# Performance work log

Measured on AMD Instinct MI355X. Metric: run time of the kernel, lower is better.

## Reference

```python
import jax, jax.numpy as jnp
import numpy as np

N_NODES = 50000
N_EDGES = 800000
H = 128
CHEM_DIM = 34   # 2 + 2*num_gdf
GEOM_DIM = 48   # 2*num_gdf + num_signatures
EPS = 1e-5


def _linear_params(key, d_in, d_out):
    kw, kb = jax.random.split(key)
    lim = 1.0 / np.sqrt(d_in)
    w = jax.random.uniform(kw, (d_in, d_out), jnp.float32, -lim, lim)
    b = jax.random.uniform(kb, (d_out,), jnp.float32, -lim, lim)
    return w, b


def setup_inputs() -> dict:
    key = jax.random.key(0)
    ks = jax.random.split(key, 16)
    inp = {
        'chem_feats': jax.random.normal(ks[0], (N_EDGES, CHEM_DIM), jnp.float32),
        'geom_feats': jax.random.normal(ks[1], (N_NODES, GEOM_DIM), jnp.float32),
        'nbr_vids': jax.random.randint(ks[2], (N_EDGES,), 0, N_NODES, jnp.int32),
    }
    # chem_mlp: Linear(34,128) -> BN(128) -> SiLU -> Linear(128,256) -> BN(256)
    inp['w_c1'], inp['b_c1'] = _linear_params(ks[3], CHEM_DIM, H)
    inp['g_c1'], inp['be_c1'] = jnp.ones((H,), jnp.float32), jnp.zeros((H,), jnp.float32)
    inp['w_c2'], inp['b_c2'] = _linear_params(ks[4], H, 2 * H)
    inp['g_c2'], inp['be_c2'] = jnp.ones((2 * H,), jnp.float32), jnp.zeros((2 * H,), jnp.float32)
    # geom_mlp: Linear(48,64) -> BN(64) -> SiLU -> Linear(64,64) -> BN(64)
    inp['w_g1'], inp['b_g1'] = _linear_params(ks[5], GEOM_DIM, H // 2)
    inp['g_g1'], inp['be_g1'] = jnp.ones((H // 2,), jnp.float32), jnp.zeros((H // 2,), jnp.float32)
    inp['w_g2'], inp['b_g2'] = _linear_params(ks[6], H // 2, H // 2)
    inp['g_g2'], inp['be_g2'] = jnp.ones((H // 2,), jnp.float32), jnp.zeros((H // 2,), jnp.float32)
    # feat_mlp: Linear(192,128) -> BN(128) -> SiLU -> Linear(128,128) -> BN(128)
    inp['w_f1'], inp['b_f1'] = _linear_params(ks[7], H + H // 2, H)
    inp['g_f1'], inp['be_f1'] = jnp.ones((H,), jnp.float32), jnp.zeros((H,), jnp.float32)
    inp['w_f2'], inp['b_f2'] = _linear_params(ks[8], H, H)
    inp['g_f2'], inp['be_f2'] = jnp.ones((H,), jnp.float32), jnp.zeros((H,), jnp.float32)
    return inp


def _bn(x, gamma, beta):
    # BatchNorm1d with batch statistics (training-mode normalization; dropout = identity at eval)
    m = jnp.mean(x, axis=0)
    v = jnp.var(x, axis=0)
    return gamma * (x - m) * jax.lax.rsqrt(v + EPS) + beta


def reference(chem_feats, geom_feats, nbr_vids,
              w_c1, b_c1, g_c1, be_c1, w_c2, b_c2, g_c2, be_c2,
              w_g1, b_g1, g_g1, be_g1, w_g2, b_g2, g_g2, be_g2,
              w_f1, b_f1, g_f1, be_f1, w_f2, b_f2, g_f2, be_f2):
    # chem branch: per-edge MLP
    h = _bn(chem_feats @ w_c1 + b_c1, g_c1, be_c1)
    h = jax.nn.silu(h)
    h = _bn(h @ w_c2 + b_c2, g_c2, be_c2)            # [E, 2H]
    nbr_filter, nbr_core = jnp.split(h, 2, axis=-1)
    h_chem = jax.nn.sigmoid(nbr_filter) * jax.nn.softplus(nbr_core)  # [E, H]
    # scatter-sum per-edge features into node bins
    h_chem = jax.ops.segment_sum(h_chem, nbr_vids, num_segments=N_NODES)  # [N, H]
    # geom branch: per-node MLP
    hg = _bn(geom_feats @ w_g1 + b_g1, g_g1, be_g1)
    hg = jax.nn.silu(hg)
    h_geom = _bn(hg @ w_g2 + b_g2, g_g2, be_g2)      # [N, H/2]
    # fuse
    hf = jnp.concatenate((h_chem, h_geom), axis=-1)  # [N, 3H/2]
    hf = _bn(hf @ w_f1 + b_f1, g_f1, be_f1)
    hf = jax.nn.silu(hf)
    h_out = _bn(hf @ w_f2 + b_f2, g_f2, be_f2)       # [N, H]
    return h_out
```

## Files before the change

### kernel.cpp

```cpp
#include <hip/hip_runtime.h>
#include <hip/hip_bf16.h>
#include <cmath>

#define E_EDGES 800000
#define N_NODES 50000
#define BN_EPS 1e-5f

typedef __attribute__((ext_vector_type(8))) short short8;
typedef __attribute__((ext_vector_type(4))) float float4v;
typedef __attribute__((ext_vector_type(4))) unsigned int uint4v;
typedef unsigned short ushort_t;

#define MFMA16(a, b, c) __builtin_amdgcn_mfma_f32_16x16x32_bf16((a), (b), (c), 0, 0, 0)

#define OFF_GX 0
#define OFF_GH 2304
#define OFF_A1 23040
#define OFF_C1 23168
#define OFF_A2 23296
#define OFF_C2 23552
#define OFF_GS1SUM 23808
#define OFF_GS1SQ 23872
#define OFF_GS2SUM 23936
#define OFF_GS2SQ 24000
#define OFF_FS1SUM 24064
#define OFF_FS1SQ 24192
#define OFF_FS2SUM 24320
#define OFF_FS2SQ 24448
#define OFF_NODE 24576
#define OFF_TG2 (OFF_NODE + N_NODES * 128)
#define OFF_TF1 (OFF_TG2 + N_NODES * 64)
#define OFF_TF2 OFF_NODE
#define OFF_W1T (OFF_TF1 + N_NODES * 128)
#define OFF_W2T (OFF_W1T + 4096)
#define OFF_BASEI (OFF_W2T + 16384)
#define OFF_BTOT (OFF_BASEI + 50176)
#define OFF_CNT (OFF_BTOT + 256)
#define OFF_CUR (OFF_CNT + 50176)
#define OFF_SIDX (OFF_CUR + 50176)
#define OFF_VIDS (OFF_SIDX + E_EDGES)
#define OFF_HLIN (OFF_VIDS + E_EDGES)

__device__ __forceinline__ float frcp_(float x) { return __builtin_amdgcn_rcpf(x); }
__device__ __forceinline__ float sigmoid_(float x) { return frcp_(1.0f + __expf(-x)); }
__device__ __forceinline__ float softplus_(float x) {
  return (x > 20.0f) ? x : __logf(1.0f + __expf(x));
}
__device__ __forceinline__ float silu_(float x) { return x * frcp_(1.0f + __expf(-x)); }

__device__ __forceinline__ ushort_t f2bf(float f) {
  __hip_bfloat16 h = __float2bfloat16(f);
  return *(ushort_t*)&h;
}
__device__ __forceinline__ float bf2f(ushort_t u) {
  return __uint_as_float(((unsigned)u) << 16);
}
__device__ __forceinline__ unsigned cvtpk(float lo, float hi) {
  unsigned r;
  asm("v_cvt_pk_bf16_f32 %0, %1, %2" : "=v"(r) : "v"(lo), "v"(hi));
  return r;
}
__device__ __forceinline__ void gload_lds16(const void* g, void* l) {
  __builtin_amdgcn_global_load_lds(
      (const __attribute__((address_space(1))) unsigned int*)g,
      (__attribute__((address_space(3))) unsigned int*)l, 16, 0, 0);
}

__device__ __forceinline__ void load_xfrag(const float* __restrict__ chem, int e, int qd,
                                           short8* x0, short8* x1) {
  const float* xe = chem + e * 34;
  float2 p0 = *(const float2*)(xe + 8 * qd);
  float2 p1 = *(const float2*)(xe + 8 * qd + 2);
  float2 p2 = *(const float2*)(xe + 8 * qd + 4);
  float2 p3 = *(const float2*)(xe + 8 * qd + 6);
  union { short8 s; uint4v u; } cv;
  cv.u[0] = cvtpk(p0.x, p0.y);
  cv.u[1] = cvtpk(p1.x, p1.y);
  cv.u[2] = cvtpk(p2.x, p2.y);
  cv.u[3] = cvtpk(p3.x, p3.y);
  *x0 = cv.s;
  union { short8 s; uint4v u; } cb;
  cb.u = (uint4v){0, 0, 0, 0};
  if (qd == 0) {
    float2 pt = *(const float2*)(xe + 32);
    cb.u[0] = cvtpk(pt.x, pt.y);
  }
  *x1 = cb.s;
}

__global__ __launch_bounds__(256) void k_prep(const float* __restrict__ w1,
                                              const float* __restrict__ w2,
                                              float* __restrict__ ws) {
  ushort_t* w1t = (ushort_t*)(ws + OFF_W1T);
  ushort_t* w2t = (ushort_t*)(ws + OFF_W2T);
  int idx = blockIdx.x * 256 + threadIdx.x;
  if (idx < 128 * 64) {
    int c = idx >> 6, k = idx & 63;
    float v = (k < 34) ? w1[k * 128 + c] : 0.0f;
    w1t[idx] = f2bf(v);
  }
  int j = idx - 128 * 64;
  if (j >= 0 && j < 256 * 128) {
    int c = j >> 7, k = j & 127;
    w2t[j] = f2bf(w2[k * 256 + c]);
  }
}

__global__ __launch_bounds__(256) void k_hist(const int* __restrict__ vids,
                                              float* __restrict__ ws) {
  const int e = blockIdx.x * 256 + threadIdx.x;
  int* cnt = (int*)(ws + OFF_CNT);
  if (e < E_EDGES) atomicAdd(&cnt[vids[e]], 1);
}

__global__ __launch_bounds__(256) void k_scan1(float* __restrict__ ws) {
  const int* cnt = (const int*)(ws + OFF_CNT);
  int* base = (int*)(ws + OFF_BASEI);
  int* btot = (int*)(ws + OFF_BTOT);
  const int t = threadIdx.x, b = blockIdx.x, i = b * 256 + t;
  const int lane = t & 63, w = t >> 6;
  int c = (i < N_NODES) ? cnt[i] : 0;
  int s = c;
#pragma unroll
  for (int o = 1; o < 64; o <<= 1) {
    int y = __shfl_up(s, o);
    if (lane >= o) s += y;
  }
  __shared__ int wsum[4];
  if (lane == 63) wsum[w] = s;
  __syncthreads();
  int add = 0;
#pragma unroll
  for (int k = 0; k < 4; ++k)
    if (k < w) add += wsum[k];
  base[i] = s + add - c;
  if (t == 255) btot[b] = s + add;
}

__global__ __launch_bounds__(256) void k_scan2(float* __restrict__ ws) {
  int* btot = (int*)(ws + OFF_BTOT);
  const int t = threadIdx.x;
  const int lane = t & 63, w = t >> 6;
  int c = (t < 196) ? btot[t] : 0;
  int s = c;
#pragma unroll
  for (int o = 1; o < 64; o <<= 1) {
    int y = __shfl_up(s, o);
    if (lane >= o) s += y;
  }
  __shared__ int wsum[4];
  if (lane == 63) wsum[w] = s;
  __syncthreads();
  int add = 0;
#pragma unroll
  for (int k = 0; k < 4; ++k)
    if (k < w) add += wsum[k];
  if (t < 196) btot[t] = s + add - c;
}

__global__ __launch_bounds__(256) void k_fill(const int* __restrict__ vids,
                                              float* __restrict__ ws) {
  const int e = blockIdx.x * 256 + threadIdx.x;
  const int* base = (const int*)(ws + OFF_BASEI);
  const int* btot = (const int*)(ws + OFF_BTOT);
  int* cur = (int*)(ws + OFF_CUR);
  int* sidx = (int*)(ws + OFF_SIDX);
  int* vsrt = (int*)(ws + OFF_VIDS);
  if (e < E_EDGES) {
    int v = vids[e];
    int pos = base[v] + btot[v >> 8] + atomicAdd(&cur[v], 1);
    sidx[pos] = e;
    vsrt[pos] = v;
  }
}

__global__ __launch_bounds__(256) void k_xstats(const float* __restrict__ chem,
                                                float* __restrict__ ws) {
  __shared__ __align__(16) ushort_t xT[2][48 * 72];
  const int t = threadIdx.x, wv = t >> 6, ln = t & 63, r15 = ln & 15, qd = ln >> 4;
  for (int i = t; i < 2 * 14 * 72; i += 256) {
    int b = i / (14 * 72), j = i % (14 * 72);
    int rr = j / 72, e = j % 72;
    xT[b][(34 + rr) * 72 + e] = (rr == 0 && e < 64) ? (ushort_t)0x3F80 : (ushort_t)0;
  }
  float4v g0 = {0, 0, 0, 0}, g1 = {0, 0, 0, 0};
#pragma unroll 2
  for (int it = 0; it < 10; ++it) {
    const int st = blockIdx.x * 10 + it;
    const int buf = it & 1;
    for (int i = t; i < 64 * 17; i += 256) {
      int e = i / 17, kp = i - e * 17;
      float2 v = *(const float2*)(chem + st * 2176 + e * 34 + 2 * kp);
      unsigned u = cvtpk(v.x, v.y);
      xT[buf][(2 * kp) * 72 + e] = (ushort_t)u;
      xT[buf][(2 * kp + 1) * 72 + e] = (ushort_t)(u >> 16);
    }
    __syncthreads();
    const ushort_t* xb = &xT[buf][0];
#pragma unroll
    for (int ks = 0; ks < 2; ++ks) {
      const ushort_t* xk = xb + ks * 32 + 8 * qd;
      short8 f0 = *(const short8*)&xk[(0 + r15) * 72];
      short8 f1 = *(const short8*)&xk[(16 + r15) * 72];
      short8 f2v = *(const short8*)&xk[(32 + r15) * 72];
      if (wv == 0) { g0 = MFMA16(f0, f0, g0); g1 = MFMA16(f0, f1, g1); }
      else if (wv == 1) { g0 = MFMA16(f0, f2v, g0); g1 = MFMA16(f1, f1, g1); }
      else if (wv == 2) { g0 = MFMA16(f1, f2v, g0); }
      else { g0 = MFMA16(f2v, f2v, g0); }
    }
  }
  float* GX = ws + OFF_GX;
  int ti0, tj0, ti1 = -1, tj1 = -1;
  if (wv == 0) { ti0 = 0; tj0 = 0; ti1 = 0; tj1 = 1; }
  else if (wv == 1) { ti0 = 0; tj0 = 2; ti1 = 1; tj1 = 1; }
  else if (wv == 2) { ti0 = 1; tj0 = 2; }
  else { ti0 = 2; tj0 = 2; }
#pragma unroll
  for (int r = 0; r < 4; ++r)
    atomicAdd(&GX[(16 * ti0 + 4 * qd + r) * 48 + 16 * tj0 + r15], g0[r]);
  if (ti1 >= 0)
#pragma unroll
    for (int r = 0; r < 4; ++r)
      atomicAdd(&GX[(16 * ti1 + 4 * qd + r) * 48 + 16 * tj1 + r15], g1[r]);
}

__global__ __launch_bounds__(64) void k_bn1(const float* __restrict__ b1,
                                            const float* __restrict__ g1,
                                            const float* __restrict__ be1,
                                            float* __restrict__ ws) {
  const int c = blockIdx.x, i = threadIdx.x;
  __shared__ float wc[34];
  const ushort_t* w1t = (const ushort_t*)(ws + OFF_W1T);
  const float* GX = ws + OFF_GX;
  if (i < 34) wc[i] = bf2f(w1t[c * 64 + i]);
  __syncthreads();
  float p = 0.0f, ps = 0.0f;
  if (i < 34) {
    float gi = 0.0f;
    for (int j = 0; j < 34; ++j) {
      int a = i, b = j;
      if ((a >> 4) > (b >> 4)) { int tt = a; a = b; b = tt; }
      gi += GX[a * 48 + b] * wc[j];
    }
    p = wc[i] * gi;
    ps = wc[i] * GX[i * 48 + 34];
  }
#pragma unroll
  for (int off = 1; off < 64; off <<= 1) {
    p += __shfl_xor(p, off);
    ps += __shfl_xor(ps, off);
  }
  if (i == 0) {
    const float E = (float)E_EDGES;
    float bc = b1[c];
    float sum = ps + E * bc;
    float sq = p + 2.0f * bc * ps + E * bc * bc;
    float m = sum / E, v = sq / E - m * m;
    float a = g1[c] * rsqrtf(v + BN_EPS);
    ws[OFF_A1 + c] = a;
    ws[OFF_C1 + c] = a * (bc - m) + be1[c];
  }
}

template <int TJA, int TJB>
__device__ __forceinline__ void ghstep(const ushort_t* hk, int r15, float4v (&g)[11]) {
  short8 f[TJB + 1];
#pragma unroll
  for (int i = 0; i <= TJB; ++i) f[i] = *(const short8*)&hk[(16 * i + r15) * 72];
  short8 f8 = *(const short8*)&hk[(128 + r15) * 72];
  int s = 0;
#pragma unroll
  for (int ti = 0; ti <= TJA; ++ti) { g[s] = MFMA16(f[ti], f[TJA], g[s]); ++s; }
  g[s] = MFMA16(f8, f[TJA], g[s]); ++s;
#pragma unroll
  for (int ti = 0; ti <= TJB; ++ti) { g[s] = MFMA16(f[ti], f[TJB], g[s]); ++s; }
  g[s] = MFMA16(f8, f[TJB], g[s]);
}

__device__ __forceinline__ void ghtile(float* GH, int ti, int tj, int r15, int qd,
                                       const float4v v) {
#pragma unroll
  for (int r = 0; r < 4; ++r)
    atomicAdd(&GH[(16 * ti + 4 * qd + r) * 144 + 16 * tj + r15], v[r]);
}

template <int TJA, int TJB>
__device__ __forceinline__ void ghflush(float* GH, int r15, int qd, const float4v (&g)[11]) {
  int s = 0;
#pragma unroll
  for (int ti = 0; ti <= TJA; ++ti) { ghtile(GH, ti, TJA, r15, qd, g[s]); ++s; }
  ghtile(GH, 8, TJA, r15, qd, g[s]); ++s;
#pragma unroll
  for (int ti = 0; ti <= TJB; ++ti) { ghtile(GH, ti, TJB, r15, qd, g[s]); ++s; }
  ghtile(GH, 8, TJB, r15, qd, g[s]);
}

__global__ __launch_bounds__(256) void k_h(const float* __restrict__ chem,
                                           float* __restrict__ ws, int store_h) {
  __shared__ __align__(16) ushort_t hT[2][144 * 72];
  const int t = threadIdx.x, wv = t >> 6, ln = t & 63, r15 = ln & 15, qd = ln >> 4;
  const ushort_t* w1t = (const ushort_t*)(ws + OFF_W1T);
  for (int i = t; i < 2 * 16 * 72; i += 256) {
    int b = i / (16 * 72), j = i % (16 * 72);
    int rr = j / 72, e = j % 72;
    hT[b][(128 + rr) * 72 + e] = (rr == 0 && e < 64) ? (ushort_t)0x3F80 : (ushort_t)0;
  }
  float a1c[2], c1c[2];
#pragma unroll
  for (int cf = 0; cf < 2; ++cf) {
    int col = 32 * wv + 16 * cf + r15;
    a1c[cf] = ws[OFF_A1 + col];
    c1c[cf] = ws[OFF_C1 + col];
  }
  float4v gacc[11];
#pragma unroll
  for (int s = 0; s < 11; ++s) gacc[s] = (float4v){0, 0, 0, 0};

#pragma unroll 2
  for (int it = 0; it < 10; ++it) {
    const int st = blockIdx.x * 10 + it;
    const int buf = it & 1;
    const int e_base = st * 64;
    short8 xa0[4], xa1[4];
#pragma unroll
    for (int rb = 0; rb < 4; ++rb)
      load_xfrag(chem, e_base + 16 * rb + r15, qd, &xa0[rb], &xa1[rb]);
#pragma unroll
    for (int cf = 0; cf < 2; ++cf) {
      const int col = 32 * wv + 16 * cf + r15;
      short8 wb0 = *(const short8*)&w1t[col * 64 + 8 * qd];
      short8 wb1 = *(const short8*)&w1t[col * 64 + 32 + 8 * qd];
#pragma unroll
      for (int rb = 0; rb < 4; ++rb) {
        float4v acc = (float4v){0, 0, 0, 0};
        acc = MFMA16(xa0[rb], wb0, acc);
        acc = MFMA16(xa1[rb], wb1, acc);
        float h0 = silu_(fmaf(a1c[cf], acc[0], c1c[cf]));
        float h1 = silu_(fmaf(a1c[cf], acc[1], c1c[cf]));
        float h2 = silu_(fmaf(a1c[cf], acc[2], c1c[cf]));
        float h3 = silu_(fmaf(a1c[cf], acc[3], c1c[cf]));
        unsigned lo = cvtpk(h0, h1), hi = cvtpk(h2, h3);
        unsigned long long pk = ((unsigned long long)hi << 32) | (unsigned long long)lo;
        *(unsigned long long*)&hT[buf][col * 72 + 16 * rb + 4 * qd] = pk;
      }
    }
    __syncthreads();
    if (store_h) {
      unsigned* hlin = (unsigned*)(ws + OFF_HLIN);
      const int e_loc = t >> 2, qq = t & 3;
      const ushort_t* hb2 = &hT[buf][0];
      unsigned* dst = hlin + (size_t)(e_base + e_loc) * 64 + 16 * qq;
#pragma unroll
      for (int jj = 0; jj < 4; ++jj) {
        uint4v o;
#pragma unroll
        for (int m = 0; m < 4; ++m) {
          int u = 16 * qq + 4 * jj + m;
          unsigned lo = hb2[(2 * u) * 72 + e_loc];
          unsigned hi = hb2[(2 * u + 1) * 72 + e_loc];
          o[m] = lo | (hi << 16);
        }
        *(uint4v*)(dst + 4 * jj) = o;
      }
    }
    const ushort_t* hb = &hT[buf][0];
#pragma unroll
    for (int ks = 0; ks < 2; ++ks) {
      const ushort_t* hk = hb + ks * 32 + 8 * qd;
      if (wv == 0) ghstep<0, 7>(hk, r15, gacc);
      else if (wv == 1) ghstep<1, 6>(hk, r15, gacc);
      else if (wv == 2) ghstep<2, 5>(hk, r15, gacc);
      else ghstep<3, 4>(hk, r15, gacc);
    }
  }
  float* GH = ws + OFF_GH;
  if (wv == 0) ghflush<0, 7>(GH, r15, qd, gacc);
  else if (wv == 1) ghflush<1, 6>(GH, r15, qd, gacc);
  else if (wv == 2) ghflush<2, 5>(GH, r15, qd, gacc);
  else ghflush<3, 4>(GH, r15, qd, gacc);
}

__global__ __launch_bounds__(128) void k_bn2(const float* __restrict__ b2,
                                             const float* __restrict__ g2,
                                             const float* __restrict__ be2,
                                             float* __restrict__ ws) {
  const int c = blockIdx.x, i = threadIdx.x;
  __shared__ float wcol[128];
  __shared__ float redQ[2], redS[2];
  const ushort_t* w2t = (const ushort_t*)(ws + OFF_W2T);
  const float* GH = ws + OFF_GH;
  wcol[i] = bf2f(w2t[c * 128 + i]);
  __syncthreads();
  float wi = wcol[i];
  float gi = 0.0f;
  for (int j = 0; j < 128; ++j) {
    int a = i, b = j;
    if ((a >> 4) > (b >> 4)) { int tt = a; a = b; b = tt; }
    gi += GH[a * 144 + b] * wcol[j];
  }
  float p = wi * gi;
  float ps = wi * GH[128 * 144 + i];
#pragma unroll
  for (int off = 1; off < 64; off <<= 1) {
    p += __shfl_xor(p, off);
    ps += __shfl_xor(ps, off);
  }
  const int wv = i >> 6, ln = i & 63;
  if (ln == 0) { redQ[wv] = p; redS[wv] = ps; }
  __syncthreads();
  if (i == 0) {
    float q = redQ[0] + redQ[1], s = redS[0] + redS[1];
    const float E = (float)E_EDGES;
    float bc = b2[c];
    float sum = s + E * bc;
    float sq = q + 2.0f * bc * s + E * bc * bc;
    float m = sum / E, v = sq / E - m * m;
    float a = g2[c] * rsqrtf(v + BN_EPS);
    ws[OFF_A2 + c] = a;
    ws[OFF_C2 + c] = a * (bc - m) + be2[c];
  }
}

__global__ __launch_bounds__(256) void k_scatter(float* __restrict__ ws) {
  __shared__ __align__(16) ushort_t hS[64 * 128];
  __shared__ __align__(16) float gS[64 * 133];
  __shared__ int vS[64];
  const int t = threadIdx.x, wv = t >> 6, ln = t & 63, r15 = ln & 15, qd = ln >> 4;
  const ushort_t* w2t = (const ushort_t*)(ws + OFF_W2T);
  const int* sidx = (const int*)(ws + OFF_SIDX);
  const int* vsrt = (const int*)(ws + OFF_VIDS);
  const unsigned* hlin = (const unsigned*)(ws + OFF_HLIN);
  float* node = ws + OFF_NODE;
  float aF2[2], cF2[2], aC2[2], cC2[2];
#pragma unroll
  for (int cf = 0; cf < 2; ++cf) {
    int col = 32 * wv + 16 * cf + r15;
    aF2[cf] = ws[OFF_A2 + col];
    cF2[cf] = ws[OFF_C2 + col];
    aC2[cf] = ws[OFF_A2 + 128 + col];
    cC2[cf] = ws[OFF_C2 + 128 + col];
  }
  const int st0 = blockIdx.x * 8;
  int eid_cur = 0, vid_cur = 0;
  if (st0 < 12500) { eid_cur = sidx[st0 * 64 + ln]; vid_cur = vsrt[st0 * 64 + ln]; }
  for (int it = 0; it < 8; ++it) {
    const int st = st0 + it;
    if (st >= 12500) break;
    int eid_nxt = 0, vid_nxt = 0;
    if (it < 7 && st + 1 < 12500) {
      eid_nxt = sidx[(st + 1) * 64 + ln];
      vid_nxt = vsrt[(st + 1) * 64 + ln];
    }
#pragma unroll
    for (int k = 0; k < 4; ++k) {
      const int row = 16 * wv + 4 * k + qd;
      const int er = __shfl(eid_cur, row);
      const int c = (ln & 15) ^ (row & 15);
      gload_lds16(hlin + (size_t)er * 64 + 4 * c, (void*)&hS[(16 * wv + 4 * k) * 128]);
    }
    __syncthreads();
    if (t < 64) vS[t] = vid_cur;
    short8 hf[4][4];
#pragma unroll
    for (int ks = 0; ks < 4; ++ks)
#pragma unroll
      for (int rb = 0; rb < 4; ++rb)
        hf[ks][rb] = *(const short8*)&hS[(16 * rb + r15) * 128 + ((4 * ks + qd) ^ r15) * 8];
#pragma unroll
    for (int cf = 0; cf < 2; ++cf) {
      const int colF = 32 * wv + 16 * cf + r15;
      float4v accF[4], accC[4];
#pragma unroll
      for (int rb = 0; rb < 4; ++rb) {
        accF[rb] = (float4v){0, 0, 0, 0};
        accC[rb] = (float4v){0, 0, 0, 0};
      }
#pragma unroll
      for (int ks = 0; ks < 4; ++ks) {
        short8 bF = *(const short8*)&w2t[colF * 128 + ks * 32 + 8 * qd];
        short8 bC = *(const short8*)&w2t[(128 + colF) * 128 + ks * 32 + 8 * qd];
#pragma unroll
        for (int rb = 0; rb < 4; ++rb) {
          accF[rb] = MFMA16(hf[ks][rb], bF, accF[rb]);
          accC[rb] = MFMA16(hf[ks][rb], bC, accC[rb]);
        }
      }
#pragma unroll
      for (int rb = 0; rb < 4; ++rb)
#pragma unroll
        for (int r = 0; r < 4; ++r) {
          float F = fmaf(aF2[cf], accF[rb][r], cF2[cf]);
          float Co = fmaf(aC2[cf], accC[rb][r], cC2[cf]);
          gS[(16 * rb + 4 * qd + r) * 133 + colF] = sigmoid_(F) * softplus_(Co);
        }
    }
    __syncthreads();
    {
      const int c = t & 127, half = t >> 7;
      const float* g = &gS[(32 * half) * 133 + c];
      const int* vv = &vS[32 * half];
      float acc = g[0];
      int vcur = vv[0];
#pragma unroll
      for (int r = 1; r < 32; ++r) {
        int v = vv[r];
        float x = g[r * 133];
        if (v != vcur) {
          atomicAdd(node + (size_t)vcur * 128 + c, acc);
          acc = 0.0f;
          vcur = v;
        }
        acc += x;
      }
      atomicAdd(node + (size_t)vcur * 128 + c, acc);
    }
    eid_cur = eid_nxt;
    vid_cur = vid_nxt;
  }
}

__global__ __launch_bounds__(256) void k_scatter_fb(const float* __restrict__ chem,
                                                    float* __restrict__ ws) {
  __shared__ __align__(16) ushort_t hS[64 * 136];
  __shared__ __align__(16) float gS[64 * 133];
  __shared__ int vS[64];
  const int t = threadIdx.x, wv = t >> 6, ln = t & 63, r15 = ln & 15, qd = ln >> 4;
  const ushort_t* w1t = (const ushort_t*)(ws + OFF_W1T);
  const ushort_t* w2t = (const ushort_t*)(ws + OFF_W2T);
  const int* sidx = (const int*)(ws + OFF_SIDX);
  const int* vsrt = (const int*)(ws + OFF_VIDS);
  float* node = ws + OFF_NODE;
  float a1c[2], c1c[2], aF2[2], cF2[2], aC2[2], cC2[2];
#pragma unroll
  for (int cf = 0; cf < 2; ++cf) {
    int col = 32 * wv + 16 * cf + r15;
    a1c[cf] = ws[OFF_A1 + col];
    c1c[cf] = ws[OFF_C1 + col];
    aF2[cf] = ws[OFF_A2 + col];
    cF2[cf] = ws[OFF_C2 + col];
    aC2[cf] = ws[OFF_A2 + 128 + col];
    cC2[cf] = ws[OFF_C2 + 128 + col];
  }
  for (int it = 0; it < 8; ++it) {
    const int st = blockIdx.x * 8 + it;
    if (st >= 12500) break;
    const int e_base = st * 64;
    const int myeid = sidx[e_base + ln];
    const int myvid = vsrt[e_base + ln];
    short8 xa0[4], xa1[4];
#pragma unroll
    for (int rb = 0; rb < 4; ++rb) {
      int er = __shfl(myeid, 16 * rb + r15);
      load_xfrag(chem, er, qd, &xa0[rb], &xa1[rb]);
    }
#pragma unroll
    for (int cf = 0; cf < 2; ++cf) {
      const int col = 32 * wv + 16 * cf + r15;
      short8 wb0 = *(const short8*)&w1t[col * 64 + 8 * qd];
      short8 wb1 = *(const short8*)&w1t[col * 64 + 32 + 8 * qd];
#pragma unroll
      for (int rb = 0; rb < 4; ++rb) {
        float4v acc = (float4v){0, 0, 0, 0};
        acc = MFMA16(xa0[rb], wb0, acc);
        acc = MFMA16(xa1[rb], wb1, acc);
#pragma unroll
        for (int r = 0; r < 4; ++r) {
          float hv = silu_(fmaf(a1c[cf], acc[r], c1c[cf]));
          hS[(16 * rb + 4 * qd + r) * 136 + col] = (ushort_t)cvtpk(hv, hv);
        }
      }
    }
    __syncthreads();
    if (t < 64) vS[t] = myvid;
#pragma unroll
    for (int cf = 0; cf < 2; ++cf) {
      const int colF = 32 * wv + 16 * cf + r15;
      float4v accF[4], accC[4];
#pragma unroll
      for (int rb = 0; rb < 4; ++rb) {
        accF[rb] = (float4v){0, 0, 0, 0};
        accC[rb] = (float4v){0, 0, 0, 0};
      }
#pragma unroll
      for (int ks = 0; ks < 4; ++ks) {
        short8 bF = *(const short8*)&w2t[colF * 128 + ks * 32 + 8 * qd];
        short8 bC = *(const short8*)&w2t[(128 + colF) * 128 + ks * 32 + 8 * qd];
#pragma unroll
        for (int rb = 0; rb < 4; ++rb) {
          short8 hf = *(const short8*)&hS[(16 * rb + r15) * 136 + ks * 32 + 8 * qd];
          accF[rb] = MFMA16(hf, bF, accF[rb]);
          accC[rb] = MFMA16(hf, bC, accC[rb]);
        }
      }
#pragma unroll
      for (int rb = 0; rb < 4; ++rb)
#pragma unroll
        for (int r = 0; r < 4; ++r) {
          float F = fmaf(aF2[cf], accF[rb][r], cF2[cf]);
          float Co = fmaf(aC2[cf], accC[rb][r], cC2[cf]);
          gS[(16 * rb + 4 * qd + r) * 133 + colF] = sigmoid_(F) * softplus_(Co);
        }
    }
    __syncthreads();
    {
      const int c = t & 127, half = t >> 7;
      const float* g = &gS[(32 * half) * 133 + c];
      const int* vv = &vS[32 * half];
      float acc = g[0];
      int vcur = vv[0];
#pragma unroll
      for (int r = 1; r < 32; ++r) {
        int v = vv[r];
        float x = g[r * 133];
        if (v != vcur) {
          atomicAdd(node + (size_t)vcur * 128 + c, acc);
          acc = 0.0f;
          vcur = v;
        }
        acc += x;
      }
      atomicAdd(node + (size_t)vcur * 128 + c, acc);
    }
  }
}

__global__ __launch_bounds__(256) void k_geom_stats1(const float* __restrict__ geom,
                                                     const float* __restrict__ wg1,
                                                     const float* __restrict__ bg1,
                                                     float* __restrict__ ws) {
  __shared__ float ssum[64], ssq[64];
  const int t = threadIdx.x, lane = t & 63, w = t >> 6;
  if (t < 64) { ssum[t] = 0.0f; ssq[t] = 0.0f; }
  __syncthreads();
  const float bcol = bg1[lane];
  const int nb = blockIdx.x * 16 + w * 4;
  float x[4], acc[4];
#pragma unroll
  for (int u = 0; u < 4; u++) {
    x[u] = (lane < 48) ? geom[(nb + u) * 48 + lane] : 0.0f;
    acc[u] = bcol;
  }
#pragma unroll 16
  for (int k = 0; k < 48; k++) {
    float wvv = wg1[k * 64 + lane];
#pragma unroll
    for (int u = 0; u < 4; u++) acc[u] = fmaf(__shfl(x[u], k), wvv, acc[u]);
  }
  float bs = 0.0f, bq = 0.0f;
#pragma unroll
  for (int u = 0; u < 4; u++) { bs += acc[u]; bq += acc[u] * acc[u]; }
  atomicAdd(&ssum[lane], bs);
  atomicAdd(&ssq[lane], bq);
  __syncthreads();
  if (t < 64) {
    atomicAdd(ws + OFF_GS1SUM + t, ssum[t]);
    atomicAdd(ws + OFF_GS1SQ + t, ssq[t]);
  }
}

__global__ __launch_bounds__(256) void k_geom_main(
    const float* __restrict__ geom, const float* __restrict__ wg1,
    const float* __restrict__ bg1, const float* __restrict__ gg1,
    const float* __restrict__ beg1, const float* __restrict__ wg2,
    const float* __restrict__ bg2, float* __restrict__ ws) {
  __shared__ float ssum[64], ssq[64];
  const int t = threadIdx.x, lane = t & 63, w = t >> 6;
  if (t < 64) { ssum[t] = 0.0f; ssq[t] = 0.0f; }
  const float invN = 1.0f / (float)N_NODES;
  float s1 = ws[OFF_GS1SUM + lane], q1 = ws[OFF_GS1SQ + lane];
  float m1 = s1 * invN, v1 = q1 * invN - m1 * m1;
  float a1 = gg1[lane] * rsqrtf(v1 + BN_EPS);
  float c1 = beg1[lane] - a1 * m1;
  const float bcol = bg1[lane], b2col = bg2[lane];
  __syncthreads();
  const int nb = blockIdx.x * 16 + w * 4;
  float x[4], tg1[4], hg[4], acc[4];
#pragma unroll
  for (int u = 0; u < 4; u++) {
    x[u] = (lane < 48) ? geom[(nb + u) * 48 + lane] : 0.0f;
    tg1[u] = bcol;
  }
#pragma unroll 16
  for (int k = 0; k < 48; k++) {
    float wvv = wg1[k * 64 + lane];
#pragma unroll
    for (int u = 0; u < 4; u++) tg1[u] = fmaf(__shfl(x[u], k), wvv, tg1[u]);
  }
#pragma unroll
  for (int u = 0; u < 4; u++) {
    hg[u] = silu_(fmaf(a1, tg1[u], c1));
    acc[u] = b2col;
  }
#pragma unroll 16
  for (int k = 0; k < 64; k++) {
    float wvv = wg2[k * 64 + lane];
#pragma unroll
    for (int u = 0; u < 4; u++) acc[u] = fmaf(__shfl(hg[u], k), wvv, acc[u]);
  }
  float bs = 0.0f, bq = 0.0f;
#pragma unroll
  for (int u = 0; u < 4; u++) {
    ws[OFF_TG2 + (nb + u) * 64 + lane] = acc[u];
    bs += acc[u]; bq += acc[u] * acc[u];
  }
  atomicAdd(&ssum[lane], bs);
  atomicAdd(&ssq[lane], bq);
  __syncthreads();
  if (t < 64) {
    atomicAdd(ws + OFF_GS2SUM + t, ssum[t]);
    atomicAdd(ws + OFF_GS2SQ + t, ssq[t]);
  }
}

__global__ __launch_bounds__(256) void k_fuse1(const float* __restrict__ wf1,
                                               const float* __restrict__ bf1,
                                               const float* __restrict__ gg2,
                                               const float* __restrict__ beg2,
                                               float* __restrict__ ws) {
  __shared__ float ssum[128], ssq[128];
  const int t = threadIdx.x, lane = t & 63, w = t >> 6;
  if (t < 128) { ssum[t] = 0.0f; ssq[t] = 0.0f; }
  const float invN = 1.0f / (float)N_NODES;
  float s2 = ws[OFF_GS2SUM + lane], q2 = ws[OFF_GS2SQ + lane];
  float mg = s2 * invN, vg = q2 * invN - mg * mg;
  float ag = gg2[lane] * rsqrtf(vg + BN_EPS);
  float cg_ = beg2[lane] - ag * mg;
  const float bA = bf1[lane], bB = bf1[64 + lane];
  __syncthreads();
  const int nb = blockIdx.x * 16 + w * 4;
  float xa[4], xb[4], xg[4], acc1[4], acc2[4];
#pragma unroll
  for (int u = 0; u < 4; u++) {
    int n = nb + u;
    xa[u] = ws[OFF_NODE + n * 128 + lane];
    xb[u] = ws[OFF_NODE + n * 128 + 64 + lane];
    xg[u] = fmaf(ag, ws[OFF_TG2 + n * 64 + lane], cg_);
    acc1[u] = bA; acc2[u] = bB;
  }
#pragma unroll 16
  for (int k = 0; k < 64; k++) {
    float w1v = wf1[k * 128 + lane], w2v = wf1[k * 128 + 64 + lane];
#pragma unroll
    for (int u = 0; u < 4; u++) {
      float xk = __shfl(xa[u], k);
      acc1[u] = fmaf(xk, w1v, acc1[u]);
      acc2[u] = fmaf(xk, w2v, acc2[u]);
    }
  }
#pragma unroll 16
  for (int k = 0; k < 64; k++) {
    float w1v = wf1[(64 + k) * 128 + lane], w2v = wf1[(64 + k) * 128 + 64 + lane];
#pragma unroll
    for (int u = 0; u < 4; u++) {
      float xk = __shfl(xb[u], k);
      acc1[u] = fmaf(xk, w1v, acc1[u]);
      acc2[u] = fmaf(xk, w2v, acc2[u]);
    }
  }
#pragma unroll 16
  for (int k = 0; k < 64; k++) {
    float w1v = wf1[(128 + k) * 128 + lane], w2v = wf1[(128 + k) * 128 + 64 + lane];
#pragma unroll
    for (int u = 0; u < 4; u++) {
      float xk = __shfl(xg[u], k);
      acc1[u] = fmaf(xk, w1v, acc1[u]);
      acc2[u] = fmaf(xk, w2v, acc2[u]);
    }
  }
  float sA = 0, qA = 0, sB = 0, qB = 0;
#pragma unroll
  for (int u = 0; u < 4; u++) {
    int n = nb + u;
    ws[OFF_TF1 + n * 128 + lane] = acc1[u];
    ws[OFF_TF1 + n * 128 + 64 + lane] = acc2[u];
    sA += acc1[u]; qA += acc1[u] * acc1[u];
    sB += acc2[u]; qB += acc2[u] * acc2[u];
  }
  atomicAdd(&ssum[lane], sA); atomicAdd(&ssq[lane], qA);
  atomicAdd(&ssum[64 + lane], sB); atomicAdd(&ssq[64 + lane], qB);
  __syncthreads();
  if (t < 128) {
    atomicAdd(ws + OFF_FS1SUM + t, ssum[t]);
    atomicAdd(ws + OFF_FS1SQ + t, ssq[t]);
  }
}

__global__ __launch_bounds__(256) void k_fuse2(const float* __restrict__ wf2,
                                               const float* __restrict__ bf2,
                                               const float* __restrict__ gf1,
                                               const float* __restrict__ bef1,
                                               float* __restrict__ ws) {
  __shared__ float ssum[128], ssq[128];
  const int t = threadIdx.x, lane = t & 63, w = t >> 6;
  if (t < 128) { ssum[t] = 0.0f; ssq[t] = 0.0f; }
  const float invN = 1.0f / (float)N_NODES;
  float sA_ = ws[OFF_FS1SUM + lane], qA_ = ws[OFF_FS1SQ + lane];
  float mA = sA_ * invN, vA = qA_ * invN - mA * mA;
  float aA = gf1[lane] * rsqrtf(vA + BN_EPS);
  float cA = bef1[lane] - aA * mA;
  float sB_ = ws[OFF_FS1SUM + 64 + lane], qB_ = ws[OFF_FS1SQ + 64 + lane];
  float mB = sB_ * invN, vB = qB_ * invN - mB * mB;
  float aB = gf1[64 + lane] * rsqrtf(vB + BN_EPS);
  float cB = bef1[64 + lane] - aB * mB;
  const float b1c = bf2[lane], b2c = bf2[64 + lane];
  __syncthreads();
  const int nb = blockIdx.x * 16 + w * 4;
  float ha[4], hb[4], acc1[4], acc2[4];
#pragma unroll
  for (int u = 0; u < 4; u++) {
    int n = nb + u;
    ha[u] = silu_(fmaf(aA, ws[OFF_TF1 + n * 128 + lane], cA));
    hb[u] = silu_(fmaf(aB, ws[OFF_TF1 + n * 128 + 64 + lane], cB));
    acc1[u] = b1c; acc2[u] = b2c;
  }
#pragma unroll 16
  for (int k = 0; k < 64; k++) {
    float w1v = wf2[k * 128 + lane], w2v = wf2[k * 128 + 64 + lane];
#pragma unroll
    for (int u = 0; u < 4; u++) {
      float xk = __shfl(ha[u], k);
      acc1[u] = fmaf(xk, w1v, acc1[u]);
      acc2[u] = fmaf(xk, w2v, acc2[u]);
    }
  }
#pragma unroll 16
  for (int k = 0; k < 64; k++) {
    float w1v = wf2[(64 + k) * 128 + lane], w2v = wf2[(64 + k) * 128 + 64 + lane];
#pragma unroll
    for (int u = 0; u < 4; u++) {
      float xk = __shfl(hb[u], k);
      acc1[u] = fmaf(xk, w1v, acc1[u]);
      acc2[u] = fmaf(xk, w2v, acc2[u]);
    }
  }
  float sA = 0, qA = 0, sB = 0, qB = 0;
#pragma unroll
  for (int u = 0; u < 4; u++) {
    int n = nb + u;
    ws[OFF_TF2 + n * 128 + lane] = acc1[u];
    ws[OFF_TF2 + n * 128 + 64 + lane] = acc2[u];
    sA += acc1[u]; qA += acc1[u] * acc1[u];
    sB += acc2[u]; qB += acc2[u] * acc2[u];
  }
  atomicAdd(&ssum[lane], sA); atomicAdd(&ssq[lane], qA);
  atomicAdd(&ssum[64 + lane], sB); atomicAdd(&ssq[64 + lane], qB);
  __syncthreads();
  if (t < 128) {
    atomicAdd(ws + OFF_FS2SUM + t, ssum[t]);
    atomicAdd(ws + OFF_FS2SQ + t, ssq[t]);
  }
}

__global__ __launch_bounds__(256) void k_final(const float* __restrict__ gf2,
                                               const float* __restrict__ bef2,
                                               const float* __restrict__ ws,
                                               float* __restrict__ out) {
  const int idx = blockIdx.x * 256 + threadIdx.x;
  const int base = idx * 4;
  if (base >= N_NODES * 128) return;
  const float invN = 1.0f / (float)N_NODES;
  const int c0 = base & 127;
  float4 v = *(const float4*)(ws + OFF_TF2 + base);
  float vv[4] = {v.x, v.y, v.z, v.w}, r[4];
#pragma unroll
  for (int j = 0; j < 4; j++) {
    int c = c0 + j;
    float s = ws[OFF_FS2SUM + c], q = ws[OFF_FS2SQ + c];
    float m = s * invN, var = q * invN - m * m;
    float a = gf2[c] * rsqrtf(var + BN_EPS);
    r[j] = fmaf(a, vv[j] - m, bef2[c]);
  }
  *(float4*)(out + base) = make_float4(r[0], r[1], r[2], r[3]);
}

extern "C" void kernel_launch(void* const* d_in, const int* in_sizes, int n_in,
                              void* d_out, int out_size, void* d_ws, size_t ws_size,
                              hipStream_t stream) {
  const float* chem = (const float*)d_in[0];
  const float* geom = (const float*)d_in[1];
  const int* vids = (const int*)d_in[2];
  const float* w_c1 = (const float*)d_in[3];  const float* b_c1 = (const float*)d_in[4];
  const float* g_c1 = (const float*)d_in[5];  const float* be_c1 = (const float*)d_in[6];
  const float* w_c2 = (const float*)d_in[7];  const float* b_c2 = (const float*)d_in[8];
  const float* g_c2 = (const float*)d_in[9];  const float* be_c2 = (const float*)d_in[10];
  const float* w_g1 = (const float*)d_in[11]; const float* b_g1 = (const float*)d_in[12];
  const float* g_g1 = (const float*)d_in[13]; const float* be_g1 = (const float*)d_in[14];
  const float* w_g2 = (const float*)d_in[15]; const float* b_g2 = (const float*)d_in[16];
  const float* g_g2 = (const float*)d_in[17]; const float* be_g2 = (const float*)d_in[18];
  const float* w_f1 = (const float*)d_in[19]; const float* b_f1 = (const float*)d_in[20];
  const float* g_f1 = (const float*)d_in[21]; const float* be_f1 = (const float*)d_in[22];
  const float* w_f2 = (const float*)d_in[23]; const float* b_f2 = (const float*)d_in[24];
  const float* g_f2 = (const float*)d_in[25]; const float* be_f2 = (const float*)d_in[26];
  float* ws = (float*)d_ws;
  float* out = (float*)d_out;

  const size_t need_ws = ((size_t)OFF_HLIN + (size_t)E_EDGES * 64) * sizeof(float);
  const int big = (ws_size >= need_ws) ? 1 : 0;

  hipMemsetAsync(d_ws, 0, (size_t)(OFF_NODE + N_NODES * 128) * sizeof(float), stream);
  hipMemsetAsync((void*)(ws + OFF_CNT), 0, (size_t)(2 * 50176) * sizeof(int), stream);

  k_prep<<<dim3(160), dim3(256), 0, stream>>>(w_c1, w_c2, ws);
  k_hist<<<dim3(3125), dim3(256), 0, stream>>>(vids, ws);
  k_scan1<<<dim3(196), dim3(256), 0, stream>>>(ws);
  k_scan2<<<dim3(1), dim3(256), 0, stream>>>(ws);
  k_fill<<<dim3(3125), dim3(256), 0, stream>>>(vids, ws);
  k_xstats<<<dim3(1250), dim3(256), 0, stream>>>(chem, ws);
  k_bn1<<<dim3(128), dim3(64), 0, stream>>>(b_c1, g_c1, be_c1, ws);
  k_h<<<dim3(1250), dim3(256), 0, stream>>>(chem, ws, big);
  k_bn2<<<dim3(256), dim3(128), 0, stream>>>(b_c2, g_c2, be_c2, ws);
  if (big) k_scatter<<<dim3(1563), dim3(256), 0, stream>>>(ws);
  else     k_scatter_fb<<<dim3(1563), dim3(256), 0, stream>>>(chem, ws);
  k_geom_stats1<<<dim3(3125), dim3(256), 0, stream>>>(geom, w_g1, b_g1, ws);
  k_geom_main<<<dim3(3125), dim3(256), 0, stream>>>(geom, w_g1, b_g1, g_g1, be_g1, w_g2, b_g2, ws);
  k_fuse1<<<dim3(3125), dim3(256), 0, stream>>>(w_f1, b_f1, g_g2, be_g2, ws);
  k_fuse2<<<dim3(3125), dim3(256), 0, stream>>>(w_f2, b_f2, g_f1, be_f1, ws);
  k_final<<<dim3(6250), dim3(256), 0, stream>>>(g_f2, be_f2, ws, out);
}
```

Measured before the change: 1.233 ms.

## Write first-layer activations in sorted order, stream them contiguously in scatter

k_h no longer stores the first-layer activations in edge order. A new k_sa kernel recomputes them from sorted edge indices and writes them in node-sorted order with an XOR-swizzled layout. k_sb then reads them with contiguous async LDS loads, double-prefetched, instead of per-edge gathers. The histogram is folded into k_xstats and k_hist is dropped. The cost is recomputing layer 1 and an extra launch and pass over the activation buffer; the gain is coalesced reads in the scatter stage and one fewer launch.

```diff
diff --git a/kernel.cpp b/kernel.cpp
--- a/kernel.cpp
+++ b/kernel.cpp
@@ -60,6 +60,11 @@
   asm("v_cvt_pk_bf16_f32 %0, %1, %2" : "=v"(r) : "v"(lo), "v"(hi));
   return r;
 }
+__device__ __forceinline__ void lds_barrier() {
+  asm volatile("s_waitcnt lgkmcnt(0)" ::: "memory");
+  __builtin_amdgcn_s_barrier();
+  asm volatile("" ::: "memory");
+}
 __device__ __forceinline__ void gload_lds16(const void* g, void* l) {
   __builtin_amdgcn_global_load_lds(
       (const __attribute__((address_space(1))) unsigned int*)g,
@@ -106,13 +111,6 @@
   }
 }
 
-__global__ __launch_bounds__(256) void k_hist(const int* __restrict__ vids,
-                                              float* __restrict__ ws) {
-  const int e = blockIdx.x * 256 + threadIdx.x;
-  int* cnt = (int*)(ws + OFF_CNT);
-  if (e < E_EDGES) atomicAdd(&cnt[vids[e]], 1);
-}
-
 __global__ __launch_bounds__(256) void k_scan1(float* __restrict__ ws) {
   const int* cnt = (const int*)(ws + OFF_CNT);
   int* base = (int*)(ws + OFF_BASEI);
@@ -175,9 +173,15 @@
 }
 
 __global__ __launch_bounds__(256) void k_xstats(const float* __restrict__ chem,
+                                                const int* __restrict__ vids,
                                                 float* __restrict__ ws) {
   __shared__ __align__(16) ushort_t xT[2][48 * 72];
   const int t = threadIdx.x, wv = t >> 6, ln = t & 63, r15 = ln & 15, qd = ln >> 4;
+  {
+    int* cnt = (int*)(ws + OFF_CNT);
+    const int e0 = blockIdx.x * 640;
+    for (int i = t; i < 640; i += 256) atomicAdd(&cnt[vids[e0 + i]], 1);
+  }
   for (int i = t; i < 2 * 14 * 72; i += 256) {
     int b = i / (14 * 72), j = i % (14 * 72);
     int rr = j / 72, e = j % 72;
@@ -296,7 +300,7 @@
 }
 
 __global__ __launch_bounds__(256) void k_h(const float* __restrict__ chem,
-                                           float* __restrict__ ws, int store_h) {
+                                           float* __restrict__ ws) {
   __shared__ __align__(16) ushort_t hT[2][144 * 72];
   const int t = threadIdx.x, wv = t >> 6, ln = t & 63, r15 = ln & 15, qd = ln >> 4;
   const ushort_t* w1t = (const ushort_t*)(ws + OFF_W1T);
@@ -345,24 +349,6 @@
       }
     }
     __syncthreads();
-    if (store_h) {
-      unsigned* hlin = (unsigned*)(ws + OFF_HLIN);
-      const int e_loc = t >> 2, qq = t & 3;
-      const ushort_t* hb2 = &hT[buf][0];
-      unsigned* dst = hlin + (size_t)(e_base + e_loc) * 64 + 16 * qq;
-#pragma unroll
-      for (int jj = 0; jj < 4; ++jj) {
-        uint4v o;
-#pragma unroll
-        for (int m = 0; m < 4; ++m) {
-          int u = 16 * qq + 4 * jj + m;
-          unsigned lo = hb2[(2 * u) * 72 + e_loc];
-          unsigned hi = hb2[(2 * u + 1) * 72 + e_loc];
-          o[m] = lo | (hi << 16);
-        }
-        *(uint4v*)(dst + 4 * jj) = o;
-      }
-    }
     const ushort_t* hb = &hT[buf][0];
 #pragma unroll
     for (int ks = 0; ks < 2; ++ks) {
@@ -421,13 +407,68 @@
   }
 }
 
-__global__ __launch_bounds__(256) void k_scatter(float* __restrict__ ws) {
+__global__ __launch_bounds__(256) void k_sa(const float* __restrict__ chem,
+                                            float* __restrict__ ws) {
+  __shared__ __align__(16) ushort_t hS[64 * 136];
+  const int t = threadIdx.x, wv = t >> 6, ln = t & 63, r15 = ln & 15, qd = ln >> 4;
+  const ushort_t* w1t = (const ushort_t*)(ws + OFF_W1T);
+  const int* sidx = (const int*)(ws + OFF_SIDX);
+  unsigned* hlin = (unsigned*)(ws + OFF_HLIN);
+  float a1c[2], c1c[2];
+#pragma unroll
+  for (int cf = 0; cf < 2; ++cf) {
+    int col = 32 * wv + 16 * cf + r15;
+    a1c[cf] = ws[OFF_A1 + col];
+    c1c[cf] = ws[OFF_C1 + col];
+  }
+  for (int it = 0; it < 4; ++it) {
+    const int st = blockIdx.x * 4 + it;
+    const int e_base = st * 64;
+    const int myeid = sidx[e_base + ln];
+    short8 xa0[4], xa1[4];
+#pragma unroll
+    for (int rb = 0; rb < 4; ++rb) {
+      int er = __shfl(myeid, 16 * rb + r15);
+      load_xfrag(chem, er, qd, &xa0[rb], &xa1[rb]);
+    }
+#pragma unroll
+    for (int cf = 0; cf < 2; ++cf) {
+      const int col = 32 * wv + 16 * cf + r15;
+      short8 wb0 = *(const short8*)&w1t[col * 64 + 8 * qd];
+      short8 wb1 = *(const short8*)&w1t[col * 64 + 32 + 8 * qd];
+#pragma unroll
+      for (int rb = 0; rb < 4; ++rb) {
+        float4v acc = (float4v){0, 0, 0, 0};
+        acc = MFMA16(xa0[rb], wb0, acc);
+        acc = MFMA16(xa1[rb], wb1, acc);
+#pragma unroll
+        for (int r = 0; r < 4; ++r) {
+          float hv = silu_(fmaf(a1c[cf], acc[r], c1c[cf]));
+          hS[(16 * rb + 4 * qd + r) * 136 + col] = (ushort_t)cvtpk(hv, hv);
+        }
+      }
+    }
+    lds_barrier();
+    {
+      const int lr = t >> 2;
+      unsigned* dst = hlin + (size_t)(e_base + lr) * 64;
+#pragma unroll
+      for (int j = 0; j < 4; ++j) {
+        const int c = 4 * (t & 3) + j;
+        uint4v v = *(const uint4v*)&hS[lr * 136 + 8 * c];
+        *(uint4v*)(dst + ((c ^ (lr & 15)) * 4)) = v;
+      }
+    }
+    lds_barrier();
+  }
+}
+
+__global__ __launch_bounds__(256) void k_sb(float* __restrict__ ws) {
   __shared__ __align__(16) ushort_t hS[64 * 128];
   __shared__ __align__(16) float gS[64 * 133];
   __shared__ int vS[64];
   const int t = threadIdx.x, wv = t >> 6, ln = t & 63, r15 = ln & 15, qd = ln >> 4;
   const ushort_t* w2t = (const ushort_t*)(ws + OFF_W2T);
-  const int* sidx = (const int*)(ws + OFF_SIDX);
   const int* vsrt = (const int*)(ws + OFF_VIDS);
   const unsigned* hlin = (const unsigned*)(ws + OFF_HLIN);
   float* node = ws + OFF_NODE;
@@ -441,31 +482,30 @@
     cC2[cf] = ws[OFF_C2 + 128 + col];
   }
   const int st0 = blockIdx.x * 8;
-  int eid_cur = 0, vid_cur = 0;
-  if (st0 < 12500) { eid_cur = sidx[st0 * 64 + ln]; vid_cur = vsrt[st0 * 64 + ln]; }
-  for (int it = 0; it < 8; ++it) {
-    const int st = st0 + it;
-    if (st >= 12500) break;
-    int eid_nxt = 0, vid_nxt = 0;
-    if (it < 7 && st + 1 < 12500) {
-      eid_nxt = sidx[(st + 1) * 64 + ln];
-      vid_nxt = vsrt[(st + 1) * 64 + ln];
-    }
-#pragma unroll
-    for (int k = 0; k < 4; ++k) {
-      const int row = 16 * wv + 4 * k + qd;
-      const int er = __shfl(eid_cur, row);
-      const int c = (ln & 15) ^ (row & 15);
-      gload_lds16(hlin + (size_t)er * 64 + 4 * c, (void*)&hS[(16 * wv + 4 * k) * 128]);
-    }
-    __syncthreads();
-    if (t < 64) vS[t] = vid_cur;
+  if (st0 >= 12500) return;
+  const int nt = (12500 - st0 < 8) ? (12500 - st0) : 8;
+#pragma unroll
+  for (int k = 0; k < 4; ++k)
+    gload_lds16(hlin + (size_t)(st0 * 64 + 16 * wv + 4 * k + (ln >> 4)) * 64 + (ln & 15) * 4,
+                (void*)&hS[(16 * wv + 4 * k) * 128]);
+  for (int it = 0; it < nt; ++it) {
+    asm volatile("s_waitcnt vmcnt(0)" ::: "memory");
+    lds_barrier();
     short8 hf[4][4];
 #pragma unroll
     for (int ks = 0; ks < 4; ++ks)
 #pragma unroll
       for (int rb = 0; rb < 4; ++rb)
         hf[ks][rb] = *(const short8*)&hS[(16 * rb + r15) * 128 + ((4 * ks + qd) ^ r15) * 8];
+    lds_barrier();
+    if (t < 64) vS[t] = vsrt[(st0 + it) * 64 + t];
+    if (it + 1 < nt) {
+      const int eb = (st0 + it + 1) * 64;
+#pragma unroll
+      for (int k = 0; k < 4; ++k)
+        gload_lds16(hlin + (size_t)(eb + 16 * wv + 4 * k + (ln >> 4)) * 64 + (ln & 15) * 4,
+                    (void*)&hS[(16 * wv + 4 * k) * 128]);
+    }
 #pragma unroll
     for (int cf = 0; cf < 2; ++cf) {
       const int colF = 32 * wv + 16 * cf + r15;
@@ -494,7 +534,7 @@
           gS[(16 * rb + 4 * qd + r) * 133 + colF] = sigmoid_(F) * softplus_(Co);
         }
     }
-    __syncthreads();
+    lds_barrier();
     {
       const int c = t & 127, half = t >> 7;
       const float* g = &gS[(32 * half) * 133 + c];
@@ -514,8 +554,6 @@
       }
       atomicAdd(node + (size_t)vcur * 128 + c, acc);
     }
-    eid_cur = eid_nxt;
-    vid_cur = vid_nxt;
   }
 }
 
@@ -901,16 +939,19 @@
   hipMemsetAsync((void*)(ws + OFF_CNT), 0, (size_t)(2 * 50176) * sizeof(int), stream);
 
   k_prep<<<dim3(160), dim3(256), 0, stream>>>(w_c1, w_c2, ws);
-  k_hist<<<dim3(3125), dim3(256), 0, stream>>>(vids, ws);
+  k_xstats<<<dim3(1250), dim3(256), 0, stream>>>(chem, vids, ws);
   k_scan1<<<dim3(196), dim3(256), 0, stream>>>(ws);
   k_scan2<<<dim3(1), dim3(256), 0, stream>>>(ws);
   k_fill<<<dim3(3125), dim3(256), 0, stream>>>(vids, ws);
-  k_xstats<<<dim3(1250), dim3(256), 0, stream>>>(chem, ws);
   k_bn1<<<dim3(128), dim3(64), 0, stream>>>(b_c1, g_c1, be_c1, ws);
-  k_h<<<dim3(1250), dim3(256), 0, stream>>>(chem, ws, big);
+  k_h<<<dim3(1250), dim3(256), 0, stream>>>(chem, ws);
   k_bn2<<<dim3(256), dim3(128), 0, stream>>>(b_c2, g_c2, be_c2, ws);
-  if (big) k_scatter<<<dim3(1563), dim3(256), 0, stream>>>(ws);
-  else     k_scatter_fb<<<dim3(1563), dim3(256), 0, stream>>>(chem, ws);
+  if (big) {
+    k_sa<<<dim3(3125), dim3(256), 0, stream>>>(chem, ws);
+    k_sb<<<dim3(1563), dim3(256), 0, stream>>>(ws);
+  } else {
+    k_scatter_fb<<<dim3(1563), dim3(256), 0, stream>>>(chem, ws);
+  }
   k_geom_stats1<<<dim3(3125), dim3(256), 0, stream>>>(geom, w_g1, b_g1, ws);
   k_geom_main<<<dim3(3125), dim3(256), 0, stream>>>(geom, w_g1, b_g1, g_g1, be_g1, w_g2, b_g2, ws);
   k_fuse1<<<dim3(3125), dim3(256), 0, stream>>>(w_f1, b_f1, g_g2, be_g2, ws);
```

After: 1.282 ms. +4.0%, slower.
